# Kernel tuning notes

Measured on AMD Instinct MI355X. Metric: run time of the kernel, lower is better.

Reference implementation:

```python
import jax, jax.numpy as jnp
import numpy as np
import math

N_NODES = 2000
LOOKBACK = 24
IN_DIM = 16
EMB_DIM = 64
BATCH = 32
LN_EPS = 1e-5


def _layernorm(v, g, b):
    mu = jnp.mean(v, axis=-1, keepdims=True)
    var = jnp.var(v, axis=-1, keepdims=True)
    return (v - mu) * jax.lax.rsqrt(var + LN_EPS) * g + b


def setup_inputs() -> dict:
    key = jax.random.key(0)
    ks = jax.random.split(key, 12)
    td = LOOKBACK * IN_DIM  # 384
    s_in = 1.0 / math.sqrt(td)
    s_d = 1.0 / math.sqrt(IN_DIM)
    return {
        "x": jax.random.normal(ks[0], (BATCH, N_NODES, LOOKBACK, IN_DIM), jnp.float32),
        "Wq": jax.random.normal(ks[1], (td, EMB_DIM), jnp.float32) * s_in,
        "bq": jax.random.normal(ks[2], (EMB_DIM,), jnp.float32) * 0.01,
        "Wk": jax.random.normal(ks[3], (td, EMB_DIM), jnp.float32) * s_in,
        "bk": jax.random.normal(ks[4], (EMB_DIM,), jnp.float32) * 0.01,
        "g0": jnp.ones((EMB_DIM,), jnp.float32),
        "beta0": jnp.zeros((EMB_DIM,), jnp.float32),
        "g1": jnp.ones((EMB_DIM,), jnp.float32),
        "beta1": jnp.zeros((EMB_DIM,), jnp.float32),
        "normal": jax.random.normal(ks[5], (N_NODES, LOOKBACK, IN_DIM), jnp.float32),
        "Win": jax.random.normal(ks[6], (IN_DIM, IN_DIM), jnp.float32) * s_d,
    }


def reference(x, Wq, bq, Wk, bk, g0, beta0, g1, beta1, normal, Win):
    b, n, t, d = x.shape
    xf = x.reshape(b, n, t * d)
    # per-sample q/k linear + layernorm (batched over b)
    q1 = _layernorm(xf @ Wq + bq, g0, beta0)  # (b, n, e)
    k1 = _layernorm(xf @ Wk + bk, g1, beta1)  # (b, n, e)
    # node-mixing attention: softmax(q k^T / sqrt(num_nodes)) @ normal
    scores = jnp.einsum('bne,bme->bnm', q1, k1) / math.sqrt(n)
    A = jax.nn.softmax(scores, axis=-1)  # (b, n, n)
    data = jnp.einsum('bnm,mf->bnf', A, normal.reshape(n, t * d)).reshape(b, n, t, d)
    # RPPsAtt attention weights over time (general attention, output_len = 1)
    query = x[:, :, -1, :] @ Win  # (b, n, d)
    att = jnp.einsum('bnd,bntd->bnt', query, data)  # scores vs context
    weight = jax.nn.softmax(att, axis=-1)  # (b, n, t)
    # res = stack(weights).permute(0,1,3,2) -> (b, n, t, 1), broadcast-add
    return data + weight[..., None]
```

## Files before the change

kernel.cpp:

```cpp
#include <hip/hip_runtime.h>
#include <math.h>

#define B_   32
#define NN   2000
#define NP   2048
#define TT   24
#define TD   384
#define EE   64
#define SCALE 0.022360679774997896f

typedef __bf16 bf16;
typedef __bf16 bf16x8 __attribute__((ext_vector_type(8)));
typedef float  f32x4  __attribute__((ext_vector_type(4)));

typedef __attribute__((address_space(3))) unsigned int       lds_u32;
typedef const __attribute__((address_space(1))) unsigned int g_u32;

__device__ __forceinline__ void dma16(const void* g, void* l) {
    __builtin_amdgcn_global_load_lds((g_u32*)g, (lds_u32*)l, 16, 0, 0);
}

__device__ __forceinline__ bool input_is_bf16(const void* g0) {
    return *reinterpret_cast<const unsigned short*>(g0) == 0x3F80;
}

__device__ __forceinline__ float safexp(float v) {
    return __expf(fminf(fmaxf(v, -30.f), 30.f));
}

__device__ __forceinline__ bf16x8 ld_frag(const bf16* p) {
    return *reinterpret_cast<const bf16x8*>(p);
}

__device__ __forceinline__ bf16x8 cvt8_f32(const float* p) {
    f32x4 a = *reinterpret_cast<const f32x4*>(p);
    f32x4 b = *reinterpret_cast<const f32x4*>(p + 4);
    bf16x8 r;
    r[0]=(bf16)a[0]; r[1]=(bf16)a[1]; r[2]=(bf16)a[2]; r[3]=(bf16)a[3];
    r[4]=(bf16)b[0]; r[5]=(bf16)b[1]; r[6]=(bf16)b[2]; r[7]=(bf16)b[3];
    return r;
}

__global__ void pack_w_k(const void* Wqv, const void* Wkv, bf16* __restrict__ Wp,
                         const void* gflag) {
    bool bf = input_is_bf16(gflag);
    int o = blockIdx.x * 256 + threadIdx.x;
    if (o >= 12*8*64*8) return;
    int j  = o & 7;
    int l  = (o >> 3) & 63;
    int nt = (o >> 9) & 7;
    int ks = o >> 12;
    int k   = ks*32 + ((l >> 4) * 8) + j;
    int col = nt*16 + (l & 15);
    float v;
    if (bf) v = (col < 64) ? (float)((const bf16*)Wqv)[k*64 + col]
                           : (float)((const bf16*)Wkv)[k*64 + col - 64];
    else    v = (col < 64) ? ((const float*)Wqv)[k*64 + col]
                           : ((const float*)Wkv)[k*64 + col - 64];
    Wp[o] = (bf16)v;
}

__global__ void pack_v_k(const void* normalv, bf16* __restrict__ Vp, const void* gflag) {
    bool bf = input_is_bf16(gflag);
    int o = blockIdx.x * 256 + threadIdx.x;
    if (o >= 64*25*512) return;
    int j  = o & 7;
    int l  = (o >> 3) & 63;
    int nt = (o >> 9) % 25;
    int kb = o / (25*512);
    int key = kb*32 + ((l >> 4) * 8) + j;
    int col = nt*16 + (l & 15);
    float v = 0.f;
    if (key < NN) {
        if (col < TD) v = bf ? (float)((const bf16*)normalv)[key*TD + col]
                             : ((const float*)normalv)[key*TD + col];
        else if (col == TD) v = 1.0f;
    }
    Vp[o] = (bf16)v;
}

__global__ void calc_query_k(const void* xv, const void* Winv, float* __restrict__ Qry,
                             const void* gflag) {
    bool bf = input_is_bf16(gflag);
    int o = blockIdx.x * 256 + threadIdx.x;
    if (o >= B_*NP*16) return;
    int d2 = o & 15;
    int n  = (o >> 4) & (NP - 1);
    int b  = o >> 15;
    float acc = 0.f;
    if (n < NN) {
        size_t xoff = ((size_t)(b*NN + n))*TD + (TT-1)*16;
        if (bf) {
            const bf16* xr = (const bf16*)xv + xoff;
            const bf16* Wn = (const bf16*)Winv;
            #pragma unroll
            for (int d = 0; d < 16; ++d) acc += (float)xr[d] * (float)Wn[d*16 + d2];
        } else {
            const float* xr = (const float*)xv + xoff;
            const float* Wn = (const float*)Winv;
            #pragma unroll
            for (int d = 0; d < 16; ++d) acc += xr[d] * Wn[d*16 + d2];
        }
    }
    Qry[o] = acc;
}

__global__ __launch_bounds__(256) void proj_ln_k(
        const void* xv, const bf16* __restrict__ Wp,
        const void* bqv, const void* bkv,
        const void* g0v, const void* be0v,
        const void* g1v, const void* be1v,
        bf16* __restrict__ Qb, bf16* __restrict__ Kp) {
    __shared__ __align__(16) bf16 Wbuf[2][4096];
    bool bf = input_is_bf16(g0v);
    int mb = blockIdx.x, b = blockIdx.y;
    int w    = threadIdx.x >> 6;
    int lane = threadIdx.x & 63;
    int quad = lane >> 4, lq = lane & 15;

    int rowA = mb*64 + w*16 + lq;
    int xrow = rowA < NN ? rowA : NN - 1;

    bf16x8 afr[12];
    if (bf) {
        const bf16* xp = (const bf16*)xv + ((size_t)(b*NN + xrow))*TD + quad*8;
        #pragma unroll
        for (int ks = 0; ks < 12; ++ks) afr[ks] = ld_frag(xp + ks*32);
    } else {
        const float* xp = (const float*)xv + ((size_t)(b*NN + xrow))*TD + quad*8;
        #pragma unroll
        for (int ks = 0; ks < 12; ++ks) afr[ks] = cvt8_f32(xp + ks*32);
    }

    auto stage = [&](int ks, int bufi) {
        const char* g = (const char*)Wp + (size_t)ks*8192;
        for (int c = w; c < 8; c += 4)
            dma16(g + c*1024 + (size_t)lane*16, &Wbuf[bufi][c*512]);
    };
    stage(0, 0);

    f32x4 acc[8];
    #pragma unroll
    for (int nt = 0; nt < 8; ++nt) acc[nt] = (f32x4){0.f, 0.f, 0.f, 0.f};
    __syncthreads();

    for (int ks = 0; ks < 12; ++ks) {
        int cur = ks & 1;
        if (ks + 1 < 12) stage(ks + 1, cur ^ 1);
        const bf16* wb = Wbuf[cur];
        #pragma unroll
        for (int nt = 0; nt < 8; ++nt) {
            bf16x8 bfr = ld_frag(wb + nt*512 + lane*8);
            acc[nt] = __builtin_amdgcn_mfma_f32_16x16x32_bf16(afr[ks], bfr, acc[nt], 0, 0, 0);
        }
        __syncthreads();
    }

    #pragma unroll
    for (int nt = 0; nt < 8; ++nt) {
        int c = nt*16 + lq;
        float bias;
        if (bf) bias = (c < 64) ? (float)((const bf16*)bqv)[c] : (float)((const bf16*)bkv)[c-64];
        else    bias = (c < 64) ? ((const float*)bqv)[c] : ((const float*)bkv)[c-64];
        #pragma unroll
        for (int r = 0; r < 4; ++r) acc[nt][r] += bias;
    }
    float outn[8][4];
    #pragma unroll
    for (int g = 0; g < 2; ++g) {
        float s[4], sq[4];
        #pragma unroll
        for (int r = 0; r < 4; ++r) {
            float p = 0.f, p2 = 0.f;
            #pragma unroll
            for (int nt = 0; nt < 4; ++nt) {
                float v = acc[g*4 + nt][r];
                p += v; p2 += v*v;
            }
            s[r] = p; sq[r] = p2;
        }
        #pragma unroll
        for (int m = 1; m < 16; m <<= 1) {
            #pragma unroll
            for (int r = 0; r < 4; ++r) {
                s[r]  += __shfl_xor(s[r],  m, 16);
                sq[r] += __shfl_xor(sq[r], m, 16);
            }
        }
        #pragma unroll
        for (int r = 0; r < 4; ++r) {
            float mean = s[r] * (1.f/64.f);
            float var  = fmaxf(sq[r] * (1.f/64.f) - mean*mean, 0.f);
            float rs   = rsqrtf(var + 1e-5f);
            #pragma unroll
            for (int nt = 0; nt < 4; ++nt) {
                int c = nt*16 + lq;
                float gv, bv;
                if (g == 0) { gv = bf ? (float)((const bf16*)g0v)[c] : ((const float*)g0v)[c];
                              bv = bf ? (float)((const bf16*)be0v)[c] : ((const float*)be0v)[c]; }
                else        { gv = bf ? (float)((const bf16*)g1v)[c] : ((const float*)g1v)[c];
                              bv = bf ? (float)((const bf16*)be1v)[c] : ((const float*)be1v)[c]; }
                outn[g*4 + nt][r] = (acc[g*4 + nt][r] - mean) * rs * gv + bv;
            }
        }
    }
    int rowq = mb*64 + w*16 + quad*4;
    #pragma unroll
    for (int r = 0; r < 4; ++r) {
        int row = rowq + r;
        bool real = row < NN;
        size_t qbase = ((size_t)(b*NP + row))*EE;
        int kb2  = row >> 5;
        int half = (row >> 4) & 1;
        int lqk  = row & 15;
        #pragma unroll
        for (int nt = 0; nt < 4; ++nt) {
            Qb[qbase + nt*16 + lq] = (bf16)(real ? outn[nt][r] : 0.f);
            int col   = nt*16 + lq;
            int f     = half*2 + (col >> 5);
            int quadk = (col >> 3) & 3;
            size_t idx = (((size_t)(b*64 + kb2)*4 + f)*64 + quadk*16 + lqk)*8 + (col & 7);
            Kp[idx] = (bf16)(real ? outn[4 + nt][r] : 0.f);
        }
    }
}

__global__ __launch_bounds__(256, 2) void attn_k(
        const bf16* __restrict__ Qb, const bf16* __restrict__ Kp,
        const bf16* __restrict__ Vp, const float* __restrict__ Qry,
        void* outv, const void* gflag) {
    __shared__ __align__(16) bf16 Kbuf[2][2048];
    __shared__ __align__(16) bf16 Vbuf[2][12800];
    __shared__ __align__(16) bf16 Pl[4][16][40];
    bool bf = input_is_bf16(gflag);
    int mb = blockIdx.x, b = blockIdx.y;
    int w    = threadIdx.x >> 6;
    int lane = threadIdx.x & 63;
    int quad = lane >> 4, lq = lane & 15;
    int rowbase = mb*64 + w*16;

    const bf16* qp = Qb + ((size_t)(b*NP + rowbase + lq))*EE + quad*8;
    bf16x8 aq0 = ld_frag(qp);
    bf16x8 aq1 = ld_frag(qp + 32);

    f32x4 acc[25];
    #pragma unroll
    for (int nt = 0; nt < 25; ++nt) acc[nt] = (f32x4){0.f, 0.f, 0.f, 0.f};

    const bf16* kg = Kp + (size_t)(b*64)*2048;
    auto stage = [&](int kb, int bufi) {
        const char* kgb = (const char*)(kg + (size_t)kb*2048);
        const char* vgb = (const char*)(Vp + (size_t)kb*12800);
        for (int c = w; c < 29; c += 4) {
            if (c < 4) dma16(kgb + c*1024 + (size_t)lane*16, &Kbuf[bufi][c*512]);
            else       dma16(vgb + (size_t)(c-4)*1024 + (size_t)lane*16, &Vbuf[bufi][(c-4)*512]);
        }
    };
    stage(0, 0);
    __syncthreads();

    for (int kb = 0; kb < 64; ++kb) {
        int cur = kb & 1;
        if (kb + 1 < 64) stage(kb + 1, cur ^ 1);
        const bf16* kc = Kbuf[cur];
        bf16x8 bk0 = ld_frag(kc + lane*8);
        bf16x8 bk1 = ld_frag(kc +  512 + lane*8);
        bf16x8 bk2 = ld_frag(kc + 1024 + lane*8);
        bf16x8 bk3 = ld_frag(kc + 1536 + lane*8);
        f32x4 s0 = (f32x4){0.f,0.f,0.f,0.f}, s1 = (f32x4){0.f,0.f,0.f,0.f};
        s0 = __builtin_amdgcn_mfma_f32_16x16x32_bf16(aq0, bk0, s0, 0, 0, 0);
        s0 = __builtin_amdgcn_mfma_f32_16x16x32_bf16(aq1, bk1, s0, 0, 0, 0);
        s1 = __builtin_amdgcn_mfma_f32_16x16x32_bf16(aq0, bk2, s1, 0, 0, 0);
        s1 = __builtin_amdgcn_mfma_f32_16x16x32_bf16(aq1, bk3, s1, 0, 0, 0);
        #pragma unroll
        for (int r = 0; r < 4; ++r) {
            Pl[w][quad*4 + r][lq]      = (bf16)safexp(s0[r] * SCALE);
            Pl[w][quad*4 + r][16 + lq] = (bf16)safexp(s1[r] * SCALE);
        }
        bf16x8 ap = ld_frag(&Pl[w][lq][quad*8]);
        const bf16* vc = Vbuf[cur];
        #pragma unroll
        for (int nt = 0; nt < 25; ++nt) {
            bf16x8 bv = ld_frag(vc + nt*512 + lane*8);
            acc[nt] = __builtin_amdgcn_mfma_f32_16x16x32_bf16(ap, bv, acc[nt], 0, 0, 0);
        }
        __syncthreads();
    }

    float inv[4];
    #pragma unroll
    for (int r = 0; r < 4; ++r) {
        float den = __shfl(acc[24][r], (lane & 48), 64);
        inv[r] = 1.f / fmaxf(den, 1e-30f);
    }
    #pragma unroll
    for (int nt = 0; nt < 24; ++nt)
        #pragma unroll
        for (int r = 0; r < 4; ++r) acc[nt][r] *= inv[r];

    float qd[4];
    #pragma unroll
    for (int r = 0; r < 4; ++r)
        qd[r] = Qry[(size_t)(b*NP + rowbase + quad*4 + r)*16 + lq];

    float dn[4] = {0.f, 0.f, 0.f, 0.f};
    #pragma unroll
    for (int t = 0; t < 24; ++t) {
        #pragma unroll
        for (int r = 0; r < 4; ++r) {
            float a = acc[t][r] * qd[r];
            a += __shfl_xor(a, 1, 16); a += __shfl_xor(a, 2, 16);
            a += __shfl_xor(a, 4, 16); a += __shfl_xor(a, 8, 16);
            dn[r] += safexp(a);
        }
    }
    #pragma unroll
    for (int r = 0; r < 4; ++r) dn[r] = 1.f / fmaxf(dn[r], 1e-30f);

    if (bf) {
        bf16* scr = &Vbuf[0][0] + w*6144;
        #pragma unroll
        for (int t = 0; t < 24; ++t) {
            #pragma unroll
            for (int r = 0; r < 4; ++r) {
                float a = acc[t][r] * qd[r];
                a += __shfl_xor(a, 1, 16); a += __shfl_xor(a, 2, 16);
                a += __shfl_xor(a, 4, 16); a += __shfl_xor(a, 8, 16);
                float wv = safexp(a) * dn[r];
                scr[(quad*4 + r)*384 + t*16 + lq] = (bf16)(acc[t][r] + wv);
            }
        }
        __syncthreads();
        if (rowbase < NN) {
            bf16* og = (bf16*)outv + ((size_t)b*NN + rowbase)*TD;
            #pragma unroll
            for (int i = 0; i < 12; ++i)
                *reinterpret_cast<bf16x8*>(og + i*512 + lane*8) =
                    *reinterpret_cast<const bf16x8*>(scr + i*512 + lane*8);
        }
    } else {
        #pragma unroll
        for (int t = 0; t < 24; ++t) {
            #pragma unroll
            for (int r = 0; r < 4; ++r) {
                float a = acc[t][r] * qd[r];
                a += __shfl_xor(a, 1, 16); a += __shfl_xor(a, 2, 16);
                a += __shfl_xor(a, 4, 16); a += __shfl_xor(a, 8, 16);
                float wv = safexp(a) * dn[r];
                int row = rowbase + quad*4 + r;
                if (row < NN)
                    ((float*)outv)[((size_t)(b*NN + row))*TD + t*16 + lq] = acc[t][r] + wv;
            }
        }
    }
}

extern "C" void kernel_launch(void* const* d_in, const int* in_sizes, int n_in,
                              void* d_out, int out_size, void* d_ws, size_t ws_size,
                              hipStream_t stream) {
    const void* x      = d_in[0];
    const void* Wq     = d_in[1];
    const void* bq     = d_in[2];
    const void* Wk     = d_in[3];
    const void* bk     = d_in[4];
    const void* g0     = d_in[5];
    const void* be0    = d_in[6];
    const void* g1     = d_in[7];
    const void* be1    = d_in[8];
    const void* normal = d_in[9];
    const void* Win    = d_in[10];

    char* ws = (char*)d_ws;
    bf16*  Qb  = (bf16*)(ws);
    bf16*  Kp  = (bf16*)(ws + 8388608);
    bf16*  Vp  = (bf16*)(ws + 16777216);
    bf16*  Wp  = (bf16*)(ws + 16777216 + 1638400);
    float* Qry = (float*)(ws + 16777216 + 1638400 + 98304);

    pack_w_k<<<dim3(192), dim3(256), 0, stream>>>(Wq, Wk, Wp, g0);
    pack_v_k<<<dim3(3200), dim3(256), 0, stream>>>(normal, Vp, g0);
    calc_query_k<<<dim3(4096), dim3(256), 0, stream>>>(x, Win, Qry, g0);
    proj_ln_k<<<dim3(32, 32), dim3(256), 0, stream>>>(x, Wp, bq, bk, g0, be0, g1, be1, Qb, Kp);
    attn_k<<<dim3(32, 32), dim3(256), 0, stream>>>(Qb, Kp, Vp, Qry, d_out, g0);
}
```

Baseline: 415.8 us.

## Process two row tiles per wave sharing V fragments, drop ones-column denominator

New measurement: 1.196 ms. 188% more time.

```diff
diff --git a/kernel.cpp b/kernel.cpp
--- a/kernel.cpp
+++ b/kernel.cpp
@@ -7,6 +7,7 @@
 #define TT   24
 #define TD   384
 #define EE   64
+#define KB_END 63
 #define SCALE 0.022360679774997896f
 
 typedef __bf16 bf16;
@@ -63,19 +64,17 @@
 __global__ void pack_v_k(const void* normalv, bf16* __restrict__ Vp, const void* gflag) {
     bool bf = input_is_bf16(gflag);
     int o = blockIdx.x * 256 + threadIdx.x;
-    if (o >= 64*25*512) return;
+    if (o >= 64*24*512) return;
     int j  = o & 7;
     int l  = (o >> 3) & 63;
-    int nt = (o >> 9) % 25;
-    int kb = o / (25*512);
+    int nt = (o >> 9) % 24;
+    int kb = o / (24*512);
     int key = kb*32 + ((l >> 4) * 8) + j;
     int col = nt*16 + (l & 15);
     float v = 0.f;
-    if (key < NN) {
-        if (col < TD) v = bf ? (float)((const bf16*)normalv)[key*TD + col]
-                             : ((const float*)normalv)[key*TD + col];
-        else if (col == TD) v = 1.0f;
-    }
+    if (key < NN)
+        v = bf ? (float)((const bf16*)normalv)[key*TD + col]
+               : ((const float*)normalv)[key*TD + col];
     Vp[o] = (bf16)v;
 }
 
@@ -229,127 +228,161 @@
         const bf16* __restrict__ Qb, const bf16* __restrict__ Kp,
         const bf16* __restrict__ Vp, const float* __restrict__ Qry,
         void* outv, const void* gflag) {
-    __shared__ __align__(16) bf16 Kbuf[2][2048];
-    __shared__ __align__(16) bf16 Vbuf[2][12800];
-    __shared__ __align__(16) bf16 Pl[4][16][40];
+    __shared__ __align__(16) bf16 Vbuf[2][12288];
+    __shared__ __align__(16) bf16 Pl[4][32][40];
     bool bf = input_is_bf16(gflag);
     int mb = blockIdx.x, b = blockIdx.y;
     int w    = threadIdx.x >> 6;
     int lane = threadIdx.x & 63;
     int quad = lane >> 4, lq = lane & 15;
-    int rowbase = mb*64 + w*16;
-
-    const bf16* qp = Qb + ((size_t)(b*NP + rowbase + lq))*EE + quad*8;
-    bf16x8 aq0 = ld_frag(qp);
-    bf16x8 aq1 = ld_frag(qp + 32);
-
-    f32x4 acc[25];
-    #pragma unroll
-    for (int nt = 0; nt < 25; ++nt) acc[nt] = (f32x4){0.f, 0.f, 0.f, 0.f};
+    int rowbase = mb*128 + w*32;
+
+    bf16x8 aq[2][2];
+    #pragma unroll
+    for (int mi = 0; mi < 2; ++mi) {
+        const bf16* qp = Qb + ((size_t)(b*NP + rowbase + mi*16 + lq))*EE + quad*8;
+        aq[mi][0] = ld_frag(qp);
+        aq[mi][1] = ld_frag(qp + 32);
+    }
+
+    f32x4 acc[2][24];
+    #pragma unroll
+    for (int mi = 0; mi < 2; ++mi)
+        #pragma unroll
+        for (int nt = 0; nt < 24; ++nt) acc[mi][nt] = (f32x4){0.f, 0.f, 0.f, 0.f};
+    float denp[2] = {0.f, 0.f};
 
     const bf16* kg = Kp + (size_t)(b*64)*2048;
-    auto stage = [&](int kb, int bufi) {
-        const char* kgb = (const char*)(kg + (size_t)kb*2048);
-        const char* vgb = (const char*)(Vp + (size_t)kb*12800);
-        for (int c = w; c < 29; c += 4) {
-            if (c < 4) dma16(kgb + c*1024 + (size_t)lane*16, &Kbuf[bufi][c*512]);
-            else       dma16(vgb + (size_t)(c-4)*1024 + (size_t)lane*16, &Vbuf[bufi][(c-4)*512]);
+    auto stageV = [&](int kb, int bufi) {
+        const char* vgb = (const char*)(Vp + (size_t)kb*12288);
+        #pragma unroll
+        for (int i = 0; i < 6; ++i) {
+            int c = w + 4*i;
+            dma16(vgb + (size_t)c*1024 + (size_t)lane*16, &Vbuf[bufi][c*512]);
         }
     };
-    stage(0, 0);
+
+    bf16x8 bk[4];
+    {
+        const bf16* kp = kg + lane*8;
+        bk[0] = ld_frag(kp); bk[1] = ld_frag(kp + 512);
+        bk[2] = ld_frag(kp + 1024); bk[3] = ld_frag(kp + 1536);
+    }
+    stageV(0, 0);
     __syncthreads();
 
-    for (int kb = 0; kb < 64; ++kb) {
+    for (int kb = 0; kb < KB_END; ++kb) {
         int cur = kb & 1;
-        if (kb + 1 < 64) stage(kb + 1, cur ^ 1);
-        const bf16* kc = Kbuf[cur];
-        bf16x8 bk0 = ld_frag(kc + lane*8);
-        bf16x8 bk1 = ld_frag(kc +  512 + lane*8);
-        bf16x8 bk2 = ld_frag(kc + 1024 + lane*8);
-        bf16x8 bk3 = ld_frag(kc + 1536 + lane*8);
-        f32x4 s0 = (f32x4){0.f,0.f,0.f,0.f}, s1 = (f32x4){0.f,0.f,0.f,0.f};
-        s0 = __builtin_amdgcn_mfma_f32_16x16x32_bf16(aq0, bk0, s0, 0, 0, 0);
-        s0 = __builtin_amdgcn_mfma_f32_16x16x32_bf16(aq1, bk1, s0, 0, 0, 0);
-        s1 = __builtin_amdgcn_mfma_f32_16x16x32_bf16(aq0, bk2, s1, 0, 0, 0);
-        s1 = __builtin_amdgcn_mfma_f32_16x16x32_bf16(aq1, bk3, s1, 0, 0, 0);
+        if (kb + 1 < KB_END) stageV(kb + 1, cur ^ 1);
+        #pragma unroll
+        for (int mi = 0; mi < 2; ++mi)
+            #pragma unroll
+            for (int nh = 0; nh < 2; ++nh) {
+                f32x4 s = (f32x4){0.f,0.f,0.f,0.f};
+                s = __builtin_amdgcn_mfma_f32_16x16x32_bf16(aq[mi][0], bk[nh*2+0], s, 0, 0, 0);
+                s = __builtin_amdgcn_mfma_f32_16x16x32_bf16(aq[mi][1], bk[nh*2+1], s, 0, 0, 0);
+                bool keyok = (kb*32 + nh*16 + lq) < NN;
+                #pragma unroll
+                for (int r = 0; r < 4; ++r) {
+                    float pv = safexp(s[r] * SCALE);
+                    Pl[w][mi*16 + quad*4 + r][nh*16 + lq] = (bf16)(keyok ? pv : 0.f);
+                }
+            }
+        if (kb + 1 < KB_END) {
+            const bf16* kp = kg + (size_t)(kb+1)*2048 + lane*8;
+            bk[0] = ld_frag(kp); bk[1] = ld_frag(kp + 512);
+            bk[2] = ld_frag(kp + 1024); bk[3] = ld_frag(kp + 1536);
+        }
+        bf16x8 ap0 = ld_frag(&Pl[w][lq][quad*8]);
+        bf16x8 ap1 = ld_frag(&Pl[w][16 + lq][quad*8]);
+        #pragma unroll
+        for (int j = 0; j < 8; ++j) { denp[0] += (float)ap0[j]; denp[1] += (float)ap1[j]; }
+        const bf16* vc = Vbuf[cur];
+        #pragma unroll
+        for (int nt = 0; nt < 24; ++nt) {
+            bf16x8 bv = ld_frag(vc + nt*512 + lane*8);
+            acc[0][nt] = __builtin_amdgcn_mfma_f32_16x16x32_bf16(ap0, bv, acc[0][nt], 0, 0, 0);
+            acc[1][nt] = __builtin_amdgcn_mfma_f32_16x16x32_bf16(ap1, bv, acc[1][nt], 0, 0, 0);
+        }
+        __syncthreads();
+    }
+
+    #pragma unroll
+    for (int mi = 0; mi < 2; ++mi) {
+        denp[mi] += __shfl_xor(denp[mi], 16);
+        denp[mi] += __shfl_xor(denp[mi], 32);
+    }
+
+    #pragma unroll
+    for (int mi = 0; mi < 2; ++mi) {
+        float inv[4];
         #pragma unroll
         for (int r = 0; r < 4; ++r) {
-            Pl[w][quad*4 + r][lq]      = (bf16)safexp(s0[r] * SCALE);
-            Pl[w][quad*4 + r][16 + lq] = (bf16)safexp(s1[r] * SCALE);
-        }
-        bf16x8 ap = ld_frag(&Pl[w][lq][quad*8]);
-        const bf16* vc = Vbuf[cur];
-        #pragma unroll
-        for (int nt = 0; nt < 25; ++nt) {
-            bf16x8 bv = ld_frag(vc + nt*512 + lane*8);
-            acc[nt] = __builtin_amdgcn_mfma_f32_16x16x32_bf16(ap, bv, acc[nt], 0, 0, 0);
-        }
-        __syncthreads();
-    }
-
-    float inv[4];
-    #pragma unroll
-    for (int r = 0; r < 4; ++r) {
-        float den = __shfl(acc[24][r], (lane & 48), 64);
-        inv[r] = 1.f / fmaxf(den, 1e-30f);
-    }
-    #pragma unroll
-    for (int nt = 0; nt < 24; ++nt)
-        #pragma unroll
-        for (int r = 0; r < 4; ++r) acc[nt][r] *= inv[r];
-
-    float qd[4];
-    #pragma unroll
-    for (int r = 0; r < 4; ++r)
-        qd[r] = Qry[(size_t)(b*NP + rowbase + quad*4 + r)*16 + lq];
-
-    float dn[4] = {0.f, 0.f, 0.f, 0.f};
-    #pragma unroll
-    for (int t = 0; t < 24; ++t) {
-        #pragma unroll
-        for (int r = 0; r < 4; ++r) {
-            float a = acc[t][r] * qd[r];
-            a += __shfl_xor(a, 1, 16); a += __shfl_xor(a, 2, 16);
-            a += __shfl_xor(a, 4, 16); a += __shfl_xor(a, 8, 16);
-            dn[r] += safexp(a);
-        }
-    }
-    #pragma unroll
-    for (int r = 0; r < 4; ++r) dn[r] = 1.f / fmaxf(dn[r], 1e-30f);
-
-    if (bf) {
-        bf16* scr = &Vbuf[0][0] + w*6144;
+            float den = __shfl(denp[mi], quad*4 + r);
+            inv[r] = 1.f / fmaxf(den, 1e-30f);
+        }
+        #pragma unroll
+        for (int nt = 0; nt < 24; ++nt)
+            #pragma unroll
+            for (int r = 0; r < 4; ++r) acc[mi][nt][r] *= inv[r];
+    }
+
+    #pragma unroll
+    for (int mi = 0; mi < 2; ++mi) {
+        int rowchunk = rowbase + mi*16;
+        float qd[4];
+        #pragma unroll
+        for (int r = 0; r < 4; ++r)
+            qd[r] = Qry[(size_t)(b*NP + rowchunk + quad*4 + r)*16 + lq];
+
+        float dn[4] = {0.f, 0.f, 0.f, 0.f};
         #pragma unroll
         for (int t = 0; t < 24; ++t) {
             #pragma unroll
             for (int r = 0; r < 4; ++r) {
-                float a = acc[t][r] * qd[r];
+                float a = acc[mi][t][r] * qd[r];
                 a += __shfl_xor(a, 1, 16); a += __shfl_xor(a, 2, 16);
                 a += __shfl_xor(a, 4, 16); a += __shfl_xor(a, 8, 16);
-                float wv = safexp(a) * dn[r];
-                scr[(quad*4 + r)*384 + t*16 + lq] = (bf16)(acc[t][r] + wv);
-            }
-        }
-        __syncthreads();
-        if (rowbase < NN) {
-            bf16* og = (bf16*)outv + ((size_t)b*NN + rowbase)*TD;
-            #pragma unroll
-            for (int i = 0; i < 12; ++i)
-                *reinterpret_cast<bf16x8*>(og + i*512 + lane*8) =
-                    *reinterpret_cast<const bf16x8*>(scr + i*512 + lane*8);
-        }
-    } else {
-        #pragma unroll
-        for (int t = 0; t < 24; ++t) {
-            #pragma unroll
-            for (int r = 0; r < 4; ++r) {
-                float a = acc[t][r] * qd[r];
-                a += __shfl_xor(a, 1, 16); a += __shfl_xor(a, 2, 16);
-                a += __shfl_xor(a, 4, 16); a += __shfl_xor(a, 8, 16);
-                float wv = safexp(a) * dn[r];
-                int row = rowbase + quad*4 + r;
-                if (row < NN)
-                    ((float*)outv)[((size_t)(b*NN + row))*TD + t*16 + lq] = acc[t][r] + wv;
+                dn[r] += safexp(a);
+            }
+        }
+        #pragma unroll
+        for (int r = 0; r < 4; ++r) dn[r] = 1.f / fmaxf(dn[r], 1e-30f);
+
+        if (bf) {
+            bf16* scr = &Vbuf[0][0] + w*6144;
+            #pragma unroll
+            for (int t = 0; t < 24; ++t) {
+                #pragma unroll
+                for (int r = 0; r < 4; ++r) {
+                    float a = acc[mi][t][r] * qd[r];
+                    a += __shfl_xor(a, 1, 16); a += __shfl_xor(a, 2, 16);
+                    a += __shfl_xor(a, 4, 16); a += __shfl_xor(a, 8, 16);
+                    float wv = safexp(a) * dn[r];
+                    scr[(quad*4 + r)*384 + t*16 + lq] = (bf16)(acc[mi][t][r] + wv);
+                }
+            }
+            if (rowchunk < NN) {
+                bf16* og = (bf16*)outv + ((size_t)b*NN + rowchunk)*TD;
+                #pragma unroll
+                for (int i = 0; i < 12; ++i)
+                    *reinterpret_cast<bf16x8*>(og + i*512 + lane*8) =
+                        *reinterpret_cast<const bf16x8*>(scr + i*512 + lane*8);
+            }
+        } else {
+            #pragma unroll
+            for (int t = 0; t < 24; ++t) {
+                #pragma unroll
+                for (int r = 0; r < 4; ++r) {
+                    float a = acc[mi][t][r] * qd[r];
+                    a += __shfl_xor(a, 1, 16); a += __shfl_xor(a, 2, 16);
+                    a += __shfl_xor(a, 4, 16); a += __shfl_xor(a, 8, 16);
+                    float wv = safexp(a) * dn[r];
+                    int row = rowchunk + quad*4 + r;
+                    if (row < NN)
+                        ((float*)outv)[((size_t)(b*NN + row))*TD + t*16 + lq] =
+                            acc[mi][t][r] + wv;
+                }
             }
         }
     }
@@ -374,12 +407,12 @@
     bf16*  Qb  = (bf16*)(ws);
     bf16*  Kp  = (bf16*)(ws + 8388608);
     bf16*  Vp  = (bf16*)(ws + 16777216);
-    bf16*  Wp  = (bf16*)(ws + 16777216 + 1638400);
-    float* Qry = (float*)(ws + 16777216 + 1638400 + 98304);
+    bf16*  Wp  = (bf16*)(ws + 18350080);
+    float* Qry = (float*)(ws + 18448384);
 
     pack_w_k<<<dim3(192), dim3(256), 0, stream>>>(Wq, Wk, Wp, g0);
-    pack_v_k<<<dim3(3200), dim3(256), 0, stream>>>(normal, Vp, g0);
+    pack_v_k<<<dim3(3072), dim3(256), 0, stream>>>(normal, Vp, g0);
     calc_query_k<<<dim3(4096), dim3(256), 0, stream>>>(x, Win, Qry, g0);
     proj_ln_k<<<dim3(32, 32), dim3(256), 0, stream>>>(x, Wp, bq, bk, g0, be0, g1, be1, Qb, Kp);
-    attn_k<<<dim3(32, 32), dim3(256), 0, stream>>>(Qb, Kp, Vp, Qry, d_out, g0);
-}
+    attn_k<<<dim3(16, 32), dim3(256), 0, stream>>>(Qb, Kp, Vp, Qry, d_out, g0);
+}
```
